# Optimization experiments

Hardware: AMD Instinct MI355X
Metric: run time of the kernel (lower is better)

Reference implementation:

```python
import jax, jax.numpy as jnp
import numpy as np
import math

H = 2048; NH = 16; HD = 128; E = 8; K = 2; F = 8192; CAP_F = 1.25
B = 2; S = 2048

def _layernorm(x, scale, bias, eps=1e-5):
    m = jnp.mean(x, axis=-1, keepdims=True)
    v = jnp.var(x, axis=-1, keepdims=True)
    return (x - m) * jax.lax.rsqrt(v + eps) * scale + bias

def _rope(x):
    # x: [B, S, NH, HD]; half-split RoPE, theta=10000
    hd = x.shape[-1]
    pos = jnp.arange(x.shape[1], dtype=jnp.float32)
    freqs = 1.0 / (10000.0 ** (jnp.arange(0, hd // 2, dtype=jnp.float32) / (hd // 2)))
    ang = pos[:, None] * freqs[None, :]              # [S, HD/2]
    cos = jnp.cos(ang)[None, :, None, :]
    sin = jnp.sin(ang)[None, :, None, :]
    x1, x2 = jnp.split(x, 2, axis=-1)
    return jnp.concatenate([x1 * cos - x2 * sin, x1 * sin + x2 * cos], axis=-1)

def setup_inputs() -> dict:
    key = jax.random.key(0)
    ks = jax.random.split(key, 16)
    std = 0.02
    inp = {
        'hidden_states': jax.random.normal(ks[0], (B, S, H), jnp.float32),
        'attention_mask': jnp.ones((B, S), jnp.int32),
        'ln1_scale': jnp.ones((H,), jnp.float32), 'ln1_bias': jnp.zeros((H,), jnp.float32),
        'ln2_scale': jnp.ones((H,), jnp.float32), 'ln2_bias': jnp.zeros((H,), jnp.float32),
        'Wq': jax.random.normal(ks[1], (H, NH * HD), jnp.float32) * std,
        'Wk': jax.random.normal(ks[2], (H, NH * HD), jnp.float32) * std,
        'Wv': jax.random.normal(ks[3], (H, NH * HD), jnp.float32) * std,
        'Wo': jax.random.normal(ks[4], (NH * HD, H), jnp.float32) * std,
        'Wg': jax.random.normal(ks[5], (H, H), jnp.float32) * std,
        'bg': jnp.zeros((H,), jnp.float32),
        'ls_attn': jnp.full((H,), 0.1, jnp.float32),
        'ls_moe': jnp.full((H,), 0.1, jnp.float32),
        'router_w': jax.random.normal(ks[6], (H, E), jnp.float32) * std,
        'W1': jax.random.normal(ks[7], (E, H, F), jnp.float32) * std,
        'b1': jnp.zeros((E, F), jnp.float32),
        'W2': jax.random.normal(ks[8], (E, F, H), jnp.float32) * std,
        'b2': jnp.zeros((E, H), jnp.float32),
    }
    return inp

def _forward(hidden_states, attention_mask, ln1_scale, ln1_bias, ln2_scale, ln2_bias,
             Wq, Wk, Wv, Wo, Wg, bg, ls_attn, ls_moe, router_w, W1, b1, W2, b2):
    b, s, h = hidden_states.shape
    # ---- pre-norm MLA attention + residual ----
    xn = _layernorm(hidden_states, ln1_scale, ln1_bias)
    q = (xn @ Wq).reshape(b, s, NH, HD)
    k = (xn @ Wk).reshape(b, s, NH, HD)
    v = (xn @ Wv).reshape(b, s, NH, HD)
    q = _rope(q); k = _rope(k)
    scores = jnp.einsum('bqhd,bkhd->bhqk', q, k) / math.sqrt(HD)
    causal = jnp.tril(jnp.ones((s, s), bool))
    mask = causal[None, None, :, :] & (attention_mask[:, None, None, :] > 0)
    scores = jnp.where(mask, scores, -1e9)
    attn = jax.nn.softmax(scores, axis=-1)
    ctx = jnp.einsum('bhqk,bkhd->bqhd', attn, v).reshape(b, s, NH * HD)
    attn_out = ctx @ Wo
    attn_out = attn_out * jax.nn.sigmoid(xn @ Wg + bg)   # output gating
    attn_out = attn_out * ls_attn                         # layer scale
    hidden_states = hidden_states + attn_out
    # ---- pre-norm MoE FFN + residual ----
    xn2 = _layernorm(hidden_states, ln2_scale, ln2_bias)
    T = b * s
    x = xn2.reshape(T, h)
    logits = (x @ router_w).astype(jnp.float32)           # [T, E]
    probs = jax.nn.softmax(logits, axis=-1)
    gates, idx = jax.lax.top_k(probs, K)                  # [T, K]
    gates = gates / jnp.sum(gates, axis=-1, keepdims=True)
    cap = int(math.ceil(T * K / E * CAP_F))               # expert capacity
    e_flat = idx.reshape(T * K)
    g_flat = gates.reshape(T * K)
    oh = jax.nn.one_hot(e_flat, E, dtype=jnp.int32)       # [TK, E]
    pos = jnp.sum(jnp.cumsum(oh, axis=0) * oh, axis=-1) - 1
    keep = (pos < cap).astype(x.dtype)
    pos_c = jnp.clip(pos, 0, cap - 1)
    x_rep = jnp.repeat(x, K, axis=0)                      # [TK, H]
    buf = jnp.zeros((E, cap, h), x.dtype).at[e_flat, pos_c].add(x_rep * keep[:, None])
    hmid = jax.nn.gelu(jnp.einsum('ech,ehf->ecf', buf, W1) + b1[:, None, :])
    obuf = jnp.einsum('ecf,efh->ech', hmid, W2) + b2[:, None, :]
    tok = obuf[e_flat, pos_c] * (keep * g_flat)[:, None]  # [TK, H]
    moe_out = tok.reshape(T, K, h).sum(axis=1).reshape(b, s, h)
    moe_out = moe_out * ls_moe
    return hidden_states + moe_out

def reference(hidden_states, attention_mask, ln1_scale, ln1_bias, ln2_scale, ln2_bias,
              Wq, Wk, Wv, Wo, Wg, bg, ls_attn, ls_moe, router_w, W1, b1, W2, b2):
    return _forward(hidden_states, attention_mask, ln1_scale, ln1_bias, ln2_scale, ln2_bias,
                    Wq, Wk, Wv, Wo, Wg, bg, ls_attn, ls_moe, router_w, W1, b1, W2, b2)
```

## Files before the change

kernel.cpp:

```cpp
#include <hip/hip_runtime.h>
#include <hip/hip_fp16.h>

typedef _Float16 f16;
typedef _Float16 half8 __attribute__((ext_vector_type(8)));
typedef float floatx4 __attribute__((ext_vector_type(4)));

constexpr int kH  = 2048;
constexpr int kS  = 2048;
constexpr int kB  = 2;
constexpr int kT  = kB * kS;
constexpr int kNH = 16;
constexpr int kHD = 128;
constexpr int kE  = 8;
constexpr int kF  = 8192;
constexpr int kCAP = 1280;
constexpr int kTK = kT * 2;

__device__ __forceinline__ void gload16(const void* g, void* lds) {
  __builtin_amdgcn_global_load_lds((const __attribute__((address_space(1))) void*)g,
                                   (__attribute__((address_space(3))) void*)lds,
                                   16, 0, 0);
}

__global__ __launch_bounds__(256) void transpose_cvt(
    const float* __restrict__ src, f16* __restrict__ dst,
    int ldS, int ldD, long sZ, long dZ)
{
  __shared__ float tile[64][65];
  src += (long)blockIdx.z * sZ;
  dst += (long)blockIdx.z * dZ;
  const int kb = blockIdx.y * 64, nb = blockIdx.x * 64;
  const int tx = threadIdx.x & 15, ty = threadIdx.x >> 4;
#pragma unroll
  for (int i = 0; i < 4; i++) {
    const int r = ty + i * 16;
    const float4 v = *(const float4*)&src[(long)(kb + r) * ldS + nb + tx * 4];
    tile[r][tx * 4 + 0] = v.x; tile[r][tx * 4 + 1] = v.y;
    tile[r][tx * 4 + 2] = v.z; tile[r][tx * 4 + 3] = v.w;
  }
  __syncthreads();
#pragma unroll
  for (int i = 0; i < 4; i++) {
    const int n = ty + i * 16;
    union { f16 h[4]; unsigned long long u; } pk;
#pragma unroll
    for (int j = 0; j < 4; j++) pk.h[j] = (f16)tile[tx * 4 + j][n];
    *(unsigned long long*)&dst[(long)(nb + n) * ldD + kb + tx * 4] = pk.u;
  }
}

__global__ __launch_bounds__(256) void ln_kernel(
    const float* __restrict__ x, const float* __restrict__ sc,
    const float* __restrict__ bi, f16* __restrict__ o16, float* __restrict__ o32)
{
  const long row = blockIdx.x;
  const float* xr = x + row * kH;
  const int t = threadIdx.x;
  const float4 u = ((const float4*)xr)[t * 2];
  const float4 v = ((const float4*)xr)[t * 2 + 1];
  float s = u.x + u.y + u.z + u.w + v.x + v.y + v.z + v.w;
  float q = u.x*u.x + u.y*u.y + u.z*u.z + u.w*u.w + v.x*v.x + v.y*v.y + v.z*v.z + v.w*v.w;
#pragma unroll
  for (int m = 1; m < 64; m <<= 1) { s += __shfl_xor(s, m); q += __shfl_xor(q, m); }
  __shared__ float red_s[4], red_q[4];
  const int w = t >> 6, l = t & 63;
  if (l == 0) { red_s[w] = s; red_q[w] = q; }
  __syncthreads();
  s = red_s[0] + red_s[1] + red_s[2] + red_s[3];
  q = red_q[0] + red_q[1] + red_q[2] + red_q[3];
  const float mean = s * (1.f / kH);
  const float var = q * (1.f / kH) - mean * mean;
  const float rstd = rsqrtf(var + 1e-5f);
  const int c = t * 8;
  const float vals[8] = {u.x, u.y, u.z, u.w, v.x, v.y, v.z, v.w};
#pragma unroll
  for (int j = 0; j < 8; j++) {
    const float y = (vals[j] - mean) * rstd * sc[c + j] + bi[c + j];
    o16[row * kH + c + j] = (f16)y;
    if (o32 != nullptr) o32[row * kH + c + j] = y;
  }
}

template <int EPI>
__global__ __launch_bounds__(256) void gemm_kernel(
    const f16* __restrict__ A, const f16* __restrict__ B, void* __restrict__ Cv,
    const float* __restrict__ bias, const int* __restrict__ rowCount,
    int M, int N, int K, long aZ, long bZ, long cZ, long biasZ)
{
  const int z = blockIdx.z;
  if (rowCount != nullptr && (int)(blockIdx.y * 128) >= rowCount[z]) return;
  __shared__ f16 As[128 * 64];
  __shared__ f16 Bs[128 * 64];
  A += (long)z * aZ;  B += (long)z * bZ;
  const int tid = threadIdx.x, w = tid >> 6, l = tid & 63;
  const int g = l >> 4, lr = l & 15;
  const long m0 = (long)blockIdx.y * 128, n0 = (long)blockIdx.x * 128;
  const int wm = (w >> 1) * 64, wn = (w & 1) * 64;
  floatx4 acc[4][4];
#pragma unroll
  for (int i = 0; i < 4; i++)
#pragma unroll
    for (int j = 0; j < 4; j++) acc[i][j] = floatx4{0.f, 0.f, 0.f, 0.f};
  const int lrow = l >> 3, lwb = (l & 7) * 16;
  const int nk = K >> 6;
  for (int kt = 0; kt < nk; kt++) {
    const long k0 = (long)kt * 64;
#pragma unroll
    for (int c = 0; c < 4; c++) {
      const int rbase = w * 32 + c * 8;
      const int row = rbase + lrow;
      const int srcoff = (lwb ^ ((row & 7) << 4)) >> 1;
      gload16(A + (m0 + row) * K + k0 + srcoff, As + rbase * 64);
      gload16(B + (n0 + row) * K + k0 + srcoff, Bs + rbase * 64);
    }
    asm volatile("s_waitcnt vmcnt(0)" ::: "memory");
    __syncthreads();
#pragma unroll
    for (int kc = 0; kc < 2; kc++) {
      half8 af[4], bf[4];
#pragma unroll
      for (int i = 0; i < 4; i++) {
        const int ra = wm + i * 16 + lr;
        af[i] = *(const half8*)((const char*)As + ra * 128 + ((kc * 64 + g * 16) ^ ((ra & 7) << 4)));
        const int rb = wn + i * 16 + lr;
        bf[i] = *(const half8*)((const char*)Bs + rb * 128 + ((kc * 64 + g * 16) ^ ((rb & 7) << 4)));
      }
#pragma unroll
      for (int mi = 0; mi < 4; mi++)
#pragma unroll
        for (int ni = 0; ni < 4; ni++)
          acc[mi][ni] = __builtin_amdgcn_mfma_f32_16x16x32_f16(af[mi], bf[ni], acc[mi][ni], 0, 0, 0);
    }
    __syncthreads();
  }
  const long crow = m0 + wm + g * 4;
  const long ccol = n0 + wn + lr;
#pragma unroll
  for (int mi = 0; mi < 4; mi++)
#pragma unroll
    for (int ni = 0; ni < 4; ni++)
#pragma unroll
      for (int j = 0; j < 4; j++) {
        const long r = crow + mi * 16 + j;
        const long c = ccol + ni * 16;
        float v = acc[mi][ni][j];
        if (EPI == 0) {
          ((float*)Cv)[(long)z * cZ + r * N + c] = v;
        } else if (EPI == 2) {
          v += bias[(long)z * biasZ + c];
          const float t2 = tanhf(0.7978845608028654f * (v + 0.044715f * v * v * v));
          ((f16*)Cv)[(long)z * cZ + r * N + c] = (f16)(0.5f * v * (1.f + t2));
        } else {
          v += bias[(long)z * biasZ + c];
          ((f16*)Cv)[(long)z * cZ + r * N + c] = (f16)v;
        }
      }
}

__global__ void rope_table_kernel(float* __restrict__ ct, float* __restrict__ st) {
  const int i = blockIdx.x * 256 + threadIdx.x;
  if (i >= kS * 64) return;
  const int s = i >> 6, f = i & 63;
  const double freq = exp(-0.14391156831212787 * (double)f);
  const double ang = (double)s * freq;
  ct[i] = (float)cos(ang);
  st[i] = (float)sin(ang);
}

__global__ __launch_bounds__(256) void rope_kernel(
    const float* __restrict__ q, const float* __restrict__ k,
    const float* __restrict__ ct, const float* __restrict__ st,
    f16* __restrict__ qr, f16* __restrict__ kr)
{
  const long t = blockIdx.x;
  const int s = (int)(t & (kS - 1)), b = (int)(t >> 11);
  for (int u = threadIdx.x; u < kNH * 64; u += 256) {
    const int h = u >> 6, i = u & 63;
    const float c = ct[s * 64 + i], sn = st[s * 64 + i];
    const long src = t * kH + h * kHD + i;
    const long dst = (((long)(b * kNH + h)) * kS + s) * kHD + i;
    float x1 = q[src], x2 = q[src + 64];
    qr[dst]      = (f16)((x1 * c - x2 * sn) * 0.08838834764831845f);
    qr[dst + 64] = (f16)((x1 * sn + x2 * c) * 0.08838834764831845f);
    x1 = k[src]; x2 = k[src + 64];
    kr[dst]      = (f16)(x1 * c - x2 * sn);
    kr[dst + 64] = (f16)(x1 * sn + x2 * c);
  }
}

__global__ __launch_bounds__(256) void attn_kernel(
    const f16* __restrict__ q_r, const f16* __restrict__ k_r,
    const f16* __restrict__ v_t, f16* __restrict__ ctx)
{
  __shared__ f16 Ks[64 * 128];
  __shared__ f16 Vs[128 * 64];
  __shared__ f16 Ps[4][1024];
  const int qt = blockIdx.x, h = blockIdx.y, b = blockIdx.z;
  const int bh = b * kNH + h;
  const int tid = threadIdx.x, w = tid >> 6, l = tid & 63;
  const int g = l >> 4, lr = l & 15;
  const long q0 = (long)qt * 64;
  const f16* qbase = q_r + ((long)bh * kS + q0 + w * 16 + lr) * kHD;
  half8 qf[4];
#pragma unroll
  for (int kc = 0; kc < 4; kc++) qf[kc] = *(const half8*)(qbase + kc * 32 + g * 8);
  floatx4 acc[8];
#pragma unroll
  for (int i = 0; i < 8; i++) acc[i] = floatx4{0.f, 0.f, 0.f, 0.f};
  float mrun[4], lrun[4];
#pragma unroll
  for (int j = 0; j < 4; j++) { mrun[j] = -1e30f; lrun[j] = 0.f; }
  f16* pw = Ps[w];

  for (int kt = 0; kt <= qt; kt++) {
    const long k0 = (long)kt * 64;
#pragma unroll
    for (int c = 0; c < 4; c++) {
      const int cc = w * 4 + c;
      const int row = cc * 4 + (l >> 4);
      const int wb = (l & 15) * 16;
      const int src = (wb ^ ((row & 7) << 4)) >> 1;
      gload16(k_r + ((long)bh * kS + k0 + row) * kHD + src, Ks + cc * 512);
    }
#pragma unroll
    for (int c = 0; c < 4; c++) {
      const int cc = w * 4 + c;
      const int row = cc * 8 + (l >> 3);
      const int wb = (l & 7) * 16;
      const int src = (wb ^ ((row & 7) << 4)) >> 1;
      gload16(v_t + ((long)bh * kHD + row) * kS + k0 + src, Vs + cc * 512);
    }
    asm volatile("s_waitcnt vmcnt(0)" ::: "memory");
    __syncthreads();

    floatx4 sfr[4];
#pragma unroll
    for (int f = 0; f < 4; f++) {
      floatx4 s4 = floatx4{0.f, 0.f, 0.f, 0.f};
      const int row = f * 16 + lr;
#pragma unroll
      for (int kc = 0; kc < 4; kc++) {
        const half8 kfq = *(const half8*)((const char*)Ks + row * 256 +
                            ((kc * 64 + g * 16) ^ ((row & 7) << 4)));
        s4 = __builtin_amdgcn_mfma_f32_16x16x32_f16(qf[kc], kfq, s4, 0, 0, 0);
      }
      sfr[f] = s4;
    }
    if (kt == qt) {
#pragma unroll
      for (int f = 0; f < 4; f++) {
        const int key = kt * 64 + f * 16 + lr;
#pragma unroll
        for (int j = 0; j < 4; j++) {
          const int qrow = qt * 64 + w * 16 + g * 4 + j;
          if (key > qrow) sfr[f][j] = -1e30f;
        }
      }
    }
    float al[4];
#pragma unroll
    for (int j = 0; j < 4; j++) {
      float pm = fmaxf(fmaxf(sfr[0][j], sfr[1][j]), fmaxf(sfr[2][j], sfr[3][j]));
      pm = fmaxf(pm, __shfl_xor(pm, 1)); pm = fmaxf(pm, __shfl_xor(pm, 2));
      pm = fmaxf(pm, __shfl_xor(pm, 4)); pm = fmaxf(pm, __shfl_xor(pm, 8));
      const float mn = fmaxf(mrun[j], pm);
      al[j] = __expf(mrun[j] - mn);
      mrun[j] = mn;
      float rs = 0.f;
#pragma unroll
      for (int f = 0; f < 4; f++) {
        const float p = __expf(sfr[f][j] - mn);
        sfr[f][j] = p; rs += p;
      }
      rs += __shfl_xor(rs, 1); rs += __shfl_xor(rs, 2);
      rs += __shfl_xor(rs, 4); rs += __shfl_xor(rs, 8);
      lrun[j] = lrun[j] * al[j] + rs;
    }
#pragma unroll
    for (int nf = 0; nf < 8; nf++)
#pragma unroll
      for (int j = 0; j < 4; j++) acc[nf][j] *= al[j];
#pragma unroll
    for (int f = 0; f < 4; f++)
#pragma unroll
      for (int j = 0; j < 4; j++) {
        const int row = g * 4 + j;
        const int byteoff = (row * 128 + (f * 16 + lr) * 2) ^ ((row & 7) << 4);
        *(f16*)((char*)pw + byteoff) = (f16)sfr[f][j];
      }
#pragma unroll
    for (int kc = 0; kc < 2; kc++) {
      const half8 pf = *(const half8*)((const char*)pw + lr * 128 +
                         ((kc * 64 + g * 16) ^ ((lr & 7) << 4)));
#pragma unroll
      for (int nf = 0; nf < 8; nf++) {
        const int vrow = nf * 16 + lr;
        const half8 vfr = *(const half8*)((const char*)Vs + vrow * 128 +
                            ((kc * 64 + g * 16) ^ ((vrow & 7) << 4)));
        acc[nf] = __builtin_amdgcn_mfma_f32_16x16x32_f16(pf, vfr, acc[nf], 0, 0, 0);
      }
    }
    __syncthreads();
  }
  const long orow = (long)b * kS + q0 + w * 16;
#pragma unroll
  for (int j = 0; j < 4; j++) {
    const float inv = 1.0f / lrun[j];
    const int r = g * 4 + j;
#pragma unroll
    for (int nf = 0; nf < 8; nf++)
      ctx[(orow + r) * kH + h * kHD + nf * 16 + lr] = (f16)(acc[nf][j] * inv);
  }
}

__global__ __launch_bounds__(256) void combine1_kernel(
    const float* __restrict__ hid, const float* __restrict__ alin,
    const float* __restrict__ glin, const float* __restrict__ bg,
    const float* __restrict__ ls, float* __restrict__ out)
{
  const long i = (long)blockIdx.x * 256 + threadIdx.x;
  const float4 hv = ((const float4*)hid)[i];
  const float4 av = ((const float4*)alin)[i];
  const float4 gv = ((const float4*)glin)[i];
  const int c = (int)(i & 511);
  const float4 lv = ((const float4*)ls)[c];
  const float4 bv = ((const float4*)bg)[c];
  float4 o;
  o.x = hv.x + lv.x * av.x / (1.f + __expf(-(gv.x + bv.x)));
  o.y = hv.y + lv.y * av.y / (1.f + __expf(-(gv.y + bv.y)));
  o.z = hv.z + lv.z * av.z / (1.f + __expf(-(gv.z + bv.z)));
  o.w = hv.w + lv.w * av.w / (1.f + __expf(-(gv.w + bv.w)));
  ((float4*)out)[i] = o;
}

__global__ __launch_bounds__(256) void router_kernel(
    const float* __restrict__ x, const float* __restrict__ rw,
    int* __restrict__ eidx, float* __restrict__ gates)
{
  const int t = blockIdx.x * 4 + (threadIdx.x >> 6);
  const int l = threadIdx.x & 63;
  const float* xr = x + (long)t * kH;
  float a[8] = {0.f, 0.f, 0.f, 0.f, 0.f, 0.f, 0.f, 0.f};
  for (int it = 0; it < kH / 64; it++) {
    const float xv = xr[it * 64 + l];
    const float* r = rw + (long)(it * 64 + l) * kE;
#pragma unroll
    for (int e = 0; e < 8; e++) a[e] += xv * r[e];
  }
#pragma unroll
  for (int e = 0; e < 8; e++)
#pragma unroll
    for (int m = 1; m < 64; m <<= 1) a[e] += __shfl_xor(a[e], m);
  if (l == 0) {
    float mx = a[0];
#pragma unroll
    for (int e = 1; e < 8; e++) mx = fmaxf(mx, a[e]);
    float p[8];
#pragma unroll
    for (int e = 0; e < 8; e++) p[e] = __expf(a[e] - mx);
    int i1 = 0; float v1 = p[0];
#pragma unroll
    for (int e = 1; e < 8; e++) if (p[e] > v1) { v1 = p[e]; i1 = e; }
    int i2 = -1; float v2 = -1.f;
#pragma unroll
    for (int e = 0; e < 8; e++) if (e != i1 && p[e] > v2) { v2 = p[e]; i2 = e; }
    const float inv = 1.f / (v1 + v2);
    eidx[t * 2] = i1; eidx[t * 2 + 1] = i2;
    gates[t * 2] = v1 * inv; gates[t * 2 + 1] = v2 * inv;
  }
}

__global__ void scan_kernel(const int* __restrict__ eidx, int* __restrict__ slot,
                            int* __restrict__ counts)
{
  const int l = threadIdx.x;
  int base[8] = {0, 0, 0, 0, 0, 0, 0, 0};
  const unsigned long long lt = (1ull << l) - 1ull;
  for (int it = 0; it < kTK / 64; it++) {
    const int i = it * 64 + l;
    const int e = eidx[i];
    int mypos = 0;
#pragma unroll
    for (int ex = 0; ex < 8; ex++) {
      const unsigned long long mk = __ballot(e == ex);
      if (e == ex) mypos = base[ex] + __popcll(mk & lt);
      base[ex] += __popcll(mk);
    }
    slot[i] = (mypos < kCAP) ? e * kCAP + mypos : -1;
  }
  if (l == 0) {
#pragma unroll
    for (int ex = 0; ex < 8; ex++) counts[ex] = min(base[ex], kCAP);
  }
}

__global__ __launch_bounds__(256) void scatter_kernel(
    const f16* __restrict__ xh, const int* __restrict__ slot, f16* __restrict__ buf)
{
  const int i = blockIdx.x;
  const int s = slot[i];
  if (s < 0) return;
  const long t = i >> 1;
  ((half8*)(buf + (long)s * kH))[threadIdx.x] =
      ((const half8*)(xh + t * kH))[threadIdx.x];
}

__global__ __launch_bounds__(256) void combine2_kernel(
    const float* __restrict__ hid2, const f16* __restrict__ obuf,
    const int* __restrict__ slot, const float* __restrict__ gates,
    const float* __restrict__ ls, float* __restrict__ out)
{
  const int t = blockIdx.x;
  const int s0 = slot[t * 2], s1 = slot[t * 2 + 1];
  const float g0 = (s0 >= 0) ? gates[t * 2] : 0.f;
  const float g1 = (s1 >= 0) ? gates[t * 2 + 1] : 0.f;
  const f16* o0 = obuf + (long)(s0 < 0 ? 0 : s0) * kH;
  const f16* o1 = obuf + (long)(s1 < 0 ? 0 : s1) * kH;
  const int c = threadIdx.x * 8;
  const float* hp = hid2 + (long)t * kH + c;
  float* op = out + (long)t * kH + c;
#pragma unroll
  for (int j = 0; j < 8; j++) {
    const float m = g0 * (float)o0[c + j] + g1 * (float)o1[c + j];
    op[j] = hp[j] + ls[c + j] * m;
  }
}

extern "C" void kernel_launch(void* const* d_in, const int* in_sizes, int n_in,
                              void* d_out, int out_size, void* d_ws, size_t ws_size,
                              hipStream_t stream)
{
  (void)in_sizes; (void)n_in;
  const float* hidden   = (const float*)d_in[0];
  const float* ln1s     = (const float*)d_in[2];
  const float* ln1b     = (const float*)d_in[3];
  const float* ln2s     = (const float*)d_in[4];
  const float* ln2b     = (const float*)d_in[5];
  const float* Wq       = (const float*)d_in[6];
  const float* Wk       = (const float*)d_in[7];
  const float* Wv       = (const float*)d_in[8];
  const float* Wo       = (const float*)d_in[9];
  const float* Wg       = (const float*)d_in[10];
  const float* bg       = (const float*)d_in[11];
  const float* ls_attn  = (const float*)d_in[12];
  const float* ls_moe   = (const float*)d_in[13];
  const float* router_w = (const float*)d_in[14];
  const float* W1       = (const float*)d_in[15];
  const float* b1       = (const float*)d_in[16];
  const float* W2       = (const float*)d_in[17];
  const float* b2       = (const float*)d_in[18];

  char* ws = (char*)d_ws;
  size_t off = 0;
  auto take = [&](size_t b) { size_t r = off; off += (b + 255) & ~(size_t)255; return r; };
  const size_t o_wT   = take(5ULL * kH * kH * 2);
  const size_t o_w1t  = take((size_t)kE * kF * kH * 2);
  const size_t o_w2t  = take((size_t)kE * kH * kF * 2);
  const size_t o_xn   = take((size_t)kT * kH * 2);
  const size_t o_qkvg = take(4ULL * kT * kH * 4);
  const size_t o_tab  = take(2ULL * kS * 64 * 4);
  const size_t o_qr   = take(3ULL * kT * kH * 2);
  const size_t o_ctx  = take((size_t)kT * kH * 2);
  const size_t o_h2   = take((size_t)kT * kH * 4);
  const size_t o_sm   = take(1 << 20);
  const size_t o_hmid = take((size_t)kE * kCAP * kF * 2);
  if (off > ws_size) { hipMemsetAsync(d_out, 0xFF, (size_t)out_size * 4, stream); return; }

  f16* wT    = (f16*)(ws + o_wT);
  f16* w1t   = (f16*)(ws + o_w1t);
  f16* w2t   = (f16*)(ws + o_w2t);
  f16* xn    = (f16*)(ws + o_xn);
  float* qf  = (float*)(ws + o_qkvg);
  float* kfp = qf + (size_t)kT * kH;
  float* vfp = kfp + (size_t)kT * kH;
  float* gfp = vfp + (size_t)kT * kH;
  float* tabc = (float*)(ws + o_tab);
  float* tabs = tabc + (size_t)kS * 64;
  f16* qr  = (f16*)(ws + o_qr);
  f16* kr  = qr + (size_t)kT * kH;
  f16* vt  = kr + (size_t)kT * kH;
  f16* ctx = (f16*)(ws + o_ctx);
  float* h2 = (float*)(ws + o_h2);
  int* eidx    = (int*)(ws + o_sm);
  float* gates = (float*)(ws + o_sm + 65536);
  int* slot    = (int*)(ws + o_sm + 131072);
  int* counts  = (int*)(ws + o_sm + 196608);
  f16* hmid = (f16*)(ws + o_hmid);
  float* attn_lin = qf;
  float* x2f = vfp;
  f16* x2h  = (f16*)(ws + o_qkvg + 1ULL * kT * kH * 4 + (size_t)kT * kH * 2);
  f16* obuf = (f16*)(ws + o_qkvg);
  f16* buf  = qr;

  const long HH = (long)kH * kH;

  transpose_cvt<<<dim3(32, 32, 1), 256, 0, stream>>>(Wq, wT + 0 * HH, kH, kH, 0, 0);
  transpose_cvt<<<dim3(32, 32, 1), 256, 0, stream>>>(Wk, wT + 1 * HH, kH, kH, 0, 0);
  transpose_cvt<<<dim3(32, 32, 1), 256, 0, stream>>>(Wv, wT + 2 * HH, kH, kH, 0, 0);
  transpose_cvt<<<dim3(32, 32, 1), 256, 0, stream>>>(Wg, wT + 3 * HH, kH, kH, 0, 0);
  transpose_cvt<<<dim3(32, 32, 1), 256, 0, stream>>>(Wo, wT + 4 * HH, kH, kH, 0, 0);
  transpose_cvt<<<dim3(kF / 64, kH / 64, kE), 256, 0, stream>>>(
      W1, w1t, kF, kH, (long)kH * kF, (long)kF * kH);
  transpose_cvt<<<dim3(kH / 64, kF / 64, kE), 256, 0, stream>>>(
      W2, w2t, kH, kF, (long)kF * kH, (long)kH * kF);
  ln_kernel<<<kT, 256, 0, stream>>>(hidden, ln1s, ln1b, xn, nullptr);
  gemm_kernel<0><<<dim3(kH / 128, kT / 128, 4), 256, 0, stream>>>(
      xn, wT, qf, nullptr, nullptr, kT, kH, kH, 0L, HH, (long)kT * kH, 0L);
  rope_table_kernel<<<(kS * 64 + 255) / 256, 256, 0, stream>>>(tabc, tabs);
  rope_kernel<<<kT, 256, 0, stream>>>(qf, kfp, tabc, tabs, qr, kr);
  for (int b = 0; b < kB; b++)
    transpose_cvt<<<dim3(kHD / 64, kS / 64, kNH), 256, 0, stream>>>(
        vfp + (size_t)b * kS * kH, vt + (size_t)b * kNH * kHD * kS,
        kH, kS, 128L, (long)kHD * kS);
  attn_kernel<<<dim3(kS / 64, kNH, kB), 256, 0, stream>>>(qr, kr, vt, ctx);
  gemm_kernel<0><<<dim3(kH / 128, kT / 128, 1), 256, 0, stream>>>(
      ctx, wT + 4 * HH, attn_lin, nullptr, nullptr, kT, kH, kH, 0L, 0L, 0L, 0L);
  combine1_kernel<<<(kT * kH / 4) / 256, 256, 0, stream>>>(
      hidden, attn_lin, gfp, bg, ls_attn, h2);
  ln_kernel<<<kT, 256, 0, stream>>>(h2, ln2s, ln2b, x2h, x2f);
  router_kernel<<<kT / 4, 256, 0, stream>>>(x2f, router_w, eidx, gates);
  scan_kernel<<<1, 64, 0, stream>>>(eidx, slot, counts);
  scatter_kernel<<<kTK, 256, 0, stream>>>(x2h, slot, buf);
  gemm_kernel<2><<<dim3(kF / 128, kCAP / 128, kE), 256, 0, stream>>>(
      buf, w1t, hmid, b1, counts, kCAP, kF, kH,
      (long)kCAP * kH, (long)kF * kH, (long)kCAP * kF, (long)kF);
  gemm_kernel<3><<<dim3(kH / 128, kCAP / 128, kE), 256, 0, stream>>>(
      hmid, w2t, obuf, b2, counts, kCAP, kH, kF,
      (long)kCAP * kF, (long)kH * kF, (long)kCAP * kH, (long)kH);
  combine2_kernel<<<kT, 256, 0, stream>>>(h2, obuf, slot, gates, ls_moe, (float*)d_out);
}
```

Measured before the change: 1.841 ms.

## Add 256x256-tile, 512-thread GEMM with 4-stage LDS pipeline for QKV and MoE

Result: slower. 1.913 ms (+3.9%).

```diff
diff --git a/kernel.cpp b/kernel.cpp
--- a/kernel.cpp
+++ b/kernel.cpp
@@ -146,10 +146,102 @@
         float v = acc[mi][ni][j];
         if (EPI == 0) {
           ((float*)Cv)[(long)z * cZ + r * N + c] = v;
+        } else {
+          v += bias[(long)z * biasZ + c];
+          ((f16*)Cv)[(long)z * cZ + r * N + c] = (f16)v;
+        }
+      }
+}
+
+template <int EPI>
+__global__ __launch_bounds__(512, 2) void gemm8_kernel(
+    const f16* __restrict__ A, const f16* __restrict__ B, void* __restrict__ Cv,
+    const float* __restrict__ bias, const int* __restrict__ rowCount,
+    int M, int N, int K, long aZ, long bZ, long cZ, long biasZ)
+{
+  const int z = blockIdx.z;
+  if (rowCount != nullptr && (int)(blockIdx.y * 256) >= rowCount[z]) return;
+  __shared__ f16 lds[4 * 16384];
+  A += (long)z * aZ;  B += (long)z * bZ;
+  const int tid = threadIdx.x, w = tid >> 6, l = tid & 63;
+  const int g = l >> 4, lr = l & 15;
+  const long m0 = (long)blockIdx.y * 256, n0 = (long)blockIdx.x * 256;
+  const int wm = (w >> 2) * 128, wn = (w & 3) * 64;
+
+  floatx4 acc[8][4];
+#pragma unroll
+  for (int i = 0; i < 8; i++)
+#pragma unroll
+    for (int j = 0; j < 4; j++) acc[i][j] = floatx4{0.f, 0.f, 0.f, 0.f};
+
+  const int srow = l >> 2;
+  const int scb  = (l & 3) * 16;
+  auto STAGE = [&](int ck) {
+    const long k0 = (long)ck * 32;
+    f16* const base = lds + (ck & 3) * 16384;
+#pragma unroll
+    for (int j = 0; j < 2; j++) {
+      const int slot = j * 8 + w;
+      const int row = slot * 16 + srow;
+      const int src = (scb ^ (((row >> 1) & 3) << 4)) >> 1;
+      gload16(A + (m0 + row) * (long)K + k0 + src, base + slot * 512);
+      gload16(B + (n0 + row) * (long)K + k0 + src, base + 8192 + slot * 512);
+    }
+  };
+
+  STAGE(0); STAGE(1); STAGE(2);
+  const int NK = K >> 5;
+  for (int i = 0; i < NK; i++) {
+    if (i + 3 < NK) STAGE(i + 3);
+    const int rem = NK - 1 - i;
+    if (rem >= 3)      asm volatile("s_waitcnt vmcnt(12)" ::: "memory");
+    else if (rem == 2) asm volatile("s_waitcnt vmcnt(8)" ::: "memory");
+    else if (rem == 1) asm volatile("s_waitcnt vmcnt(4)" ::: "memory");
+    else               asm volatile("s_waitcnt vmcnt(0)" ::: "memory");
+    __builtin_amdgcn_s_barrier();
+    __builtin_amdgcn_sched_barrier(0);
+
+    const char* cb = (const char*)lds + (i & 3) * 32768;
+    half8 af[8], bf[4];
+#pragma unroll
+    for (int mi = 0; mi < 8; mi++) {
+      const int r = wm + mi * 16 + lr;
+      af[mi] = *(const half8*)(cb + r * 64 + ((g * 16) ^ (((r >> 1) & 3) << 4)));
+    }
+#pragma unroll
+    for (int ni = 0; ni < 4; ni++) {
+      const int r = wn + ni * 16 + lr;
+      bf[ni] = *(const half8*)(cb + 16384 + r * 64 + ((g * 16) ^ (((r >> 1) & 3) << 4)));
+    }
+    __builtin_amdgcn_s_setprio(1);
+#pragma unroll
+    for (int mi = 0; mi < 8; mi++)
+#pragma unroll
+      for (int ni = 0; ni < 4; ni++)
+        acc[mi][ni] = __builtin_amdgcn_mfma_f32_16x16x32_f16(af[mi], bf[ni], acc[mi][ni], 0, 0, 0);
+    __builtin_amdgcn_s_setprio(0);
+    __builtin_amdgcn_sched_barrier(0);
+    __builtin_amdgcn_s_barrier();
+  }
+
+  const long crow = m0 + wm + g * 4;
+  const long ccol = n0 + wn + lr;
+#pragma unroll
+  for (int mi = 0; mi < 8; mi++)
+#pragma unroll
+    for (int ni = 0; ni < 4; ni++)
+#pragma unroll
+      for (int j = 0; j < 4; j++) {
+        const long r = crow + mi * 16 + j;
+        const long c = ccol + ni * 16;
+        float v = acc[mi][ni][j];
+        if (EPI == 0) {
+          ((float*)Cv)[(long)z * cZ + r * N + c] = v;
         } else if (EPI == 2) {
           v += bias[(long)z * biasZ + c];
-          const float t2 = tanhf(0.7978845608028654f * (v + 0.044715f * v * v * v));
-          ((f16*)Cv)[(long)z * cZ + r * N + c] = (f16)(0.5f * v * (1.f + t2));
+          const float u2 = 1.5957691216057308f * (v + 0.044715f * v * v * v);
+          const float sg = 1.f / (1.f + __expf(-u2));
+          ((f16*)Cv)[(long)z * cZ + r * N + c] = (f16)(v * sg);
         } else {
           v += bias[(long)z * biasZ + c];
           ((f16*)Cv)[(long)z * cZ + r * N + c] = (f16)v;
@@ -504,7 +596,7 @@
   transpose_cvt<<<dim3(kH / 64, kF / 64, kE), 256, 0, stream>>>(
       W2, w2t, kH, kF, (long)kF * kH, (long)kH * kF);
   ln_kernel<<<kT, 256, 0, stream>>>(hidden, ln1s, ln1b, xn, nullptr);
-  gemm_kernel<0><<<dim3(kH / 128, kT / 128, 4), 256, 0, stream>>>(
+  gemm8_kernel<0><<<dim3(kH / 256, kT / 256, 4), 512, 0, stream>>>(
       xn, wT, qf, nullptr, nullptr, kT, kH, kH, 0L, HH, (long)kT * kH, 0L);
   rope_table_kernel<<<(kS * 64 + 255) / 256, 256, 0, stream>>>(tabc, tabs);
   rope_kernel<<<kT, 256, 0, stream>>>(qf, kfp, tabc, tabs, qr, kr);
@@ -521,10 +613,10 @@
   router_kernel<<<kT / 4, 256, 0, stream>>>(x2f, router_w, eidx, gates);
   scan_kernel<<<1, 64, 0, stream>>>(eidx, slot, counts);
   scatter_kernel<<<kTK, 256, 0, stream>>>(x2h, slot, buf);
-  gemm_kernel<2><<<dim3(kF / 128, kCAP / 128, kE), 256, 0, stream>>>(
+  gemm8_kernel<2><<<dim3(kF / 256, kCAP / 256, kE), 512, 0, stream>>>(
       buf, w1t, hmid, b1, counts, kCAP, kF, kH,
       (long)kCAP * kH, (long)kF * kH, (long)kCAP * kF, (long)kF);
-  gemm_kernel<3><<<dim3(kH / 128, kCAP / 128, kE), 256, 0, stream>>>(
+  gemm8_kernel<3><<<dim3(kH / 256, kCAP / 256, kE), 512, 0, stream>>>(
       hmid, w2t, obuf, b2, counts, kCAP, kH, kF,
       (long)kCAP * kF, (long)kH * kF, (long)kCAP * kH, (long)kH);
   combine2_kernel<<<kT, 256, 0, stream>>>(h2, obuf, slot, gates, ls_moe, (float*)d_out);
```
